# Performance work log

Hardware: AMD Instinct MI355X
Metric: run time of the kernel (lower is better)

## Reference

```python
import math
import jax, jax.numpy as jnp
import numpy as np

B, S, D, H, HD = 2, 2048, 1024, 16, 64  # batch, seq, dim, heads, head_dim
EPS = 1e-5

def setup_inputs() -> dict:
    key = jax.random.key(0)
    ks = jax.random.split(key, 10)
    init = lambda k, shape: jax.random.normal(k, shape, jnp.float32) * 0.02
    return {
        "x": jax.random.normal(ks[0], (B, S, D), jnp.float32),
        "cos": jax.random.uniform(ks[1], (1, S, 1, 1, HD), dtype=jnp.float32),
        "sin": jax.random.uniform(ks[2], (1, S, 1, 1, HD), dtype=jnp.float32),
        "c": jax.random.normal(ks[3], (B, D), jnp.float32),
        "norm1_w": jnp.ones((D,), jnp.float32),
        "w_qkv": init(ks[4], (3 * D, D)),
        "w_out": init(ks[5], (D, D)),
        "norm2_w": jnp.ones((D,), jnp.float32),
        "mlp_w1": init(ks[6], (4 * D, D)),
        "mlp_b1": jnp.zeros((4 * D,), jnp.float32),
        "mlp_w2": init(ks[7], (D, 4 * D)),
        "mlp_b2": jnp.zeros((D,), jnp.float32),
        "ada_w": init(ks[8], (6 * D, D)),
        "ada_b": init(ks[9], (6 * D,)),
    }

def _ln(x, w):
    # LayerNorm computed in fp32, no bias, then scaled by weight
    xf = x.astype(jnp.float32)
    mu = xf.mean(-1, keepdims=True)
    var = xf.var(-1, keepdims=True)
    return (xf - mu) * jax.lax.rsqrt(var + EPS) * w

def _modulate(h, shift, scale):
    return h * (1.0 + scale[:, None, :]) + shift[:, None, :]

def reference(x, cos, sin, c, norm1_w, w_qkv, w_out, norm2_w,
              mlp_w1, mlp_b1, mlp_w2, mlp_b2, ada_w, ada_b):
    # adaLN modulation params: [B, 6D] -> six [B, D] chunks
    ada = c @ ada_w.T + ada_b
    sh_msa, sc_msa, g_msa, sh_mlp, sc_mlp, g_mlp = jnp.split(ada, 6, axis=-1)

    # attention branch (flash_attn path: no rotary applied, naive full softmax)
    h = _modulate(_ln(x, norm1_w), sh_msa, sc_msa)
    qkv = (h @ w_qkv.T).reshape(B, S, 3, H, HD)
    q, k, v = qkv[:, :, 0], qkv[:, :, 1], qkv[:, :, 2]
    scores = jnp.einsum('bqhd,bkhd->bhqk', q, k) / math.sqrt(HD)
    probs = jax.nn.softmax(scores, axis=-1)
    attn = jnp.einsum('bhqk,bkhd->bqhd', probs, v).reshape(B, S, D)
    # gate * dropout(out) + residual; eval mode -> dropout = identity
    x = x + g_msa[:, None, :] * (attn @ w_out.T)

    # MLP branch
    h = _modulate(_ln(x, norm2_w), sh_mlp, sc_mlp)
    h = jax.nn.gelu(h @ mlp_w1.T + mlp_b1, approximate=True) @ mlp_w2.T + mlp_b2
    return x + g_mlp[:, None, :] * h
```

## Files before the change

### kernel.cpp

```cpp
#include <hip/hip_runtime.h>
#include <stdint.h>

typedef __attribute__((ext_vector_type(4))) float f32x4;
typedef __attribute__((ext_vector_type(8))) __bf16 bf16x8;

#define DEV static __device__ __forceinline__

DEV unsigned short f2bf(float f){
    uint32_t u = __float_as_uint(f);
    u += 0x7FFFu + ((u >> 16) & 1u);
    return (unsigned short)(u >> 16);
}
DEV float bf2f(unsigned short s){
    uint32_t u = ((uint32_t)s) << 16;
    return __uint_as_float(u);
}

typedef __attribute__((address_space(1))) const void as1v;
typedef __attribute__((address_space(3))) void as3v;
DEV void g2l16(const void* g, void* l){
    __builtin_amdgcn_global_load_lds((as1v*)g, (as3v*)l, 16, 0, 0);
}

__global__ __launch_bounds__(256) void k_cast_bf16(const float* __restrict__ in,
                                                   unsigned short* __restrict__ out, int n4){
    int i = blockIdx.x * 256 + threadIdx.x;
    if (i < n4){
        float4 v = ((const float4*)in)[i];
        ((ushort4*)out)[i] = make_ushort4(f2bf(v.x), f2bf(v.y), f2bf(v.z), f2bf(v.w));
    }
}

__global__ __launch_bounds__(256) void k_ada(const float* __restrict__ c,
                                             const float* __restrict__ aw,
                                             const float* __restrict__ ab,
                                             float* __restrict__ out){
    int wid  = blockIdx.x * 4 + (threadIdx.x >> 6);
    int lane = threadIdx.x & 63;
    int b = wid / 6144, r = wid % 6144;
    const float4* cw = (const float4*)(c + (size_t)b * 1024);
    const float4* wr = (const float4*)(aw + (size_t)r * 1024);
    float s = 0.f;
    #pragma unroll
    for (int i = 0; i < 4; i++){
        float4 a = wr[lane + i * 64];
        float4 q = cw[lane + i * 64];
        s += a.x*q.x + a.y*q.y + a.z*q.z + a.w*q.w;
    }
    #pragma unroll
    for (int off = 32; off > 0; off >>= 1) s += __shfl_down(s, off);
    if (lane == 0) out[wid] = s + ab[r];
}

__global__ __launch_bounds__(256) void k_ln_mod(const float* __restrict__ x,
                                                const float* __restrict__ w,
                                                const float* __restrict__ ada,
                                                int sh_off, int sc_off,
                                                unsigned short* __restrict__ out){
    int row = blockIdx.x;
    int b   = row >> 11;
    int tid = threadIdx.x;
    float4 v = ((const float4*)(x + (size_t)row * 1024))[tid];
    float s  = v.x + v.y + v.z + v.w;
    float ss = v.x*v.x + v.y*v.y + v.z*v.z + v.w*v.w;
    #pragma unroll
    for (int off = 32; off > 0; off >>= 1){ s += __shfl_down(s, off); ss += __shfl_down(ss, off); }
    __shared__ float red[8];
    int wv = tid >> 6;
    if ((tid & 63) == 0){ red[wv] = s; red[4 + wv] = ss; }
    __syncthreads();
    float S  = red[0] + red[1] + red[2] + red[3];
    float SS = red[4] + red[5] + red[6] + red[7];
    float mu   = S * (1.f / 1024.f);
    float rstd = rsqrtf(SS * (1.f / 1024.f) - mu * mu + 1e-5f);
    const float* adab = ada + (size_t)b * 6144;
    float4 wv4 = ((const float4*)w)[tid];
    float4 sh  = ((const float4*)(adab + sh_off))[tid];
    float4 sc  = ((const float4*)(adab + sc_off))[tid];
    float h0 = (v.x - mu) * rstd * wv4.x * (1.f + sc.x) + sh.x;
    float h1 = (v.y - mu) * rstd * wv4.y * (1.f + sc.y) + sh.y;
    float h2 = (v.z - mu) * rstd * wv4.z * (1.f + sc.z) + sh.z;
    float h3 = (v.w - mu) * rstd * wv4.w * (1.f + sc.w) + sh.w;
    ((ushort4*)(out + (size_t)row * 1024))[tid] = make_ushort4(f2bf(h0), f2bf(h1), f2bf(h2), f2bf(h3));
}

template<int MODE>
__global__ __launch_bounds__(256) void k_gemm(const unsigned short* __restrict__ A,
                                              const unsigned short* __restrict__ B,
                                              void* __restrict__ outp,
                                              const float* __restrict__ bias,
                                              const float* __restrict__ res,
                                              const float* __restrict__ ada, int goff,
                                              int M, int N, int K){
    __shared__ unsigned short As[2 * 128 * 32];
    __shared__ unsigned short Bs[2 * 128 * 32];
    int tid = threadIdx.x, lane = tid & 63, wv = tid >> 6;
    int quad = lane >> 4, l15 = lane & 15;
    int wm = wv & 1, wn = wv >> 1;
    int bm = blockIdx.x, bn = blockIdx.y;
    int klo, khi;
    if constexpr (MODE == 3){
        klo = blockIdx.z * 1376;
        khi = klo + 1376; if (khi > K) khi = K;
    } else {
        int kpb = K / gridDim.z;
        klo = blockIdx.z * kpb; khi = klo + kpb;
    }
    f32x4 acc[4][4] = {};
    int srow = wv * 16 + (lane >> 2), sseg = lane & 3;
    const unsigned short* ga = A + (size_t)(bm * 128 + srow) * K + sseg * 8;
    const unsigned short* gb = B + (size_t)(bn * 128 + srow) * K + sseg * 8;
    size_t stride64 = (size_t)64 * K;
    int wb = wv * 512;
    g2l16(ga + klo,            As + wb);
    g2l16(ga + stride64 + klo, As + 2048 + wb);
    g2l16(gb + klo,            Bs + wb);
    g2l16(gb + stride64 + klo, Bs + 2048 + wb);
    for (int k0 = klo; k0 < khi; k0 += 32){
        int cur = ((k0 - klo) >> 5) & 1;
        unsigned short* as = As + cur * 4096;
        unsigned short* bs = Bs + cur * 4096;
        __syncthreads();
        if (k0 + 32 < khi){
            unsigned short* an = As + (cur ^ 1) * 4096;
            unsigned short* bn = Bs + (cur ^ 1) * 4096;
            g2l16(ga + k0 + 32,            an + wb);
            g2l16(ga + stride64 + k0 + 32, an + 2048 + wb);
            g2l16(gb + k0 + 32,            bn + wb);
            g2l16(gb + stride64 + k0 + 32, bn + 2048 + wb);
        }
        bf16x8 af[4], bfr[4];
        #pragma unroll
        for (int i = 0; i < 4; i++)
            af[i] = *(const bf16x8*)(as + (wm * 64 + i * 16 + l15) * 32 + quad * 8);
        #pragma unroll
        for (int j = 0; j < 4; j++)
            bfr[j] = *(const bf16x8*)(bs + (wn * 64 + j * 16 + l15) * 32 + quad * 8);
        #pragma unroll
        for (int i = 0; i < 4; i++)
            #pragma unroll
            for (int j = 0; j < 4; j++)
                acc[i][j] = __builtin_amdgcn_mfma_f32_16x16x32_bf16(af[i], bfr[j], acc[i][j], 0, 0, 0);
    }
    unsigned short* zp = nullptr;
    if constexpr (MODE == 3){
        int z = blockIdx.z;
        if (z < 2) zp = (unsigned short*)outp + (size_t)z * 4194304;
        else       zp = (unsigned short*)(void*)bias;
    }
    int row0 = bm * 128 + wm * 64, col0 = bn * 128 + wn * 64;
    #pragma unroll
    for (int i = 0; i < 4; i++){
        #pragma unroll
        for (int r = 0; r < 4; r++){
            int row = row0 + i * 16 + quad * 4 + r;
            #pragma unroll
            for (int j = 0; j < 4; j++){
                int col = col0 + j * 16 + l15;
                float v = acc[i][j][r];
                size_t idx = (size_t)row * N + col;
                if constexpr (MODE == 0){
                    ((unsigned short*)outp)[idx] = f2bf(v);
                } else if constexpr (MODE == 1){
                    float t = v + bias[col];
                    float u = 1.5957691216057308f * (t + 0.044715f * t * t * t);
                    float g = t / (1.f + __expf(-u));
                    ((unsigned short*)outp)[idx] = f2bf(g);
                } else if constexpr (MODE == 2){
                    float t = v;
                    if (bias) t += bias[col];
                    int bb = row >> 11;
                    float g = ada[(size_t)bb * 6144 + goff + col];
                    ((float*)outp)[idx] = res[idx] + g * t;
                } else {
                    zp[idx] = f2bf(v);
                }
            }
        }
    }
}

__global__ __launch_bounds__(256) void k_ep2(const unsigned short* __restrict__ z01,
                                             const unsigned short* __restrict__ z2,
                                             const float* __restrict__ bias,
                                             const float* __restrict__ res,
                                             const float* __restrict__ ada, int goff,
                                             float* __restrict__ out){
    int row = blockIdx.x;
    int bb  = row >> 11;
    int tid = threadIdx.x;
    size_t base = (size_t)row * 1024 + tid * 4;
    ushort4 a0 = *(const ushort4*)(z01 + base);
    ushort4 a1 = *(const ushort4*)(z01 + 4194304 + base);
    ushort4 a2 = *(const ushort4*)(z2 + base);
    float4 rv = *(const float4*)(res + base);
    float4 bv = ((const float4*)bias)[tid];
    float4 gv = ((const float4*)(ada + (size_t)bb * 6144 + goff))[tid];
    float4 o;
    o.x = rv.x + gv.x * (bf2f(a0.x) + bf2f(a1.x) + bf2f(a2.x) + bv.x);
    o.y = rv.y + gv.y * (bf2f(a0.y) + bf2f(a1.y) + bf2f(a2.y) + bv.y);
    o.z = rv.z + gv.z * (bf2f(a0.z) + bf2f(a1.z) + bf2f(a2.z) + bv.z);
    o.w = rv.w + gv.w * (bf2f(a0.w) + bf2f(a1.w) + bf2f(a2.w) + bv.w);
    *(float4*)(out + base) = o;
}

__global__ __launch_bounds__(256) void k_vt(const unsigned short* __restrict__ qkv,
                                            unsigned short* __restrict__ vt){
    __shared__ unsigned short T[64 * 66];
    int kb = blockIdx.x, bh = blockIdx.y;
    int b = bh >> 4, h = bh & 15;
    size_t rb = (size_t)b * 2048;
    int t = threadIdx.x;
    int key = t >> 2, seg = t & 3;
    const unsigned short* src = qkv + (rb + kb * 64 + key) * 3072 + 2048 + h * 64;
    uint4 v0 = *(const uint4*)(src + seg * 8);
    uint4 v1 = *(const uint4*)(src + 32 + seg * 8);
    const unsigned short* p0 = (const unsigned short*)&v0;
    const unsigned short* p1 = (const unsigned short*)&v1;
    unsigned short* tr = T + key * 66;
    ushort2* t0 = (ushort2*)(tr + seg * 8);
    ushort2* t1 = (ushort2*)(tr + 32 + seg * 8);
    #pragma unroll
    for (int j = 0; j < 4; j++){
        t0[j] = make_ushort2(p0[2*j], p0[2*j+1]);
        t1[j] = make_ushort2(p1[2*j], p1[2*j+1]);
    }
    __syncthreads();
    int d = t >> 2, kseg = t & 3;
    unsigned short obuf[16];
    #pragma unroll
    for (int j = 0; j < 16; j++) obuf[j] = T[(kseg * 16 + j) * 66 + d];
    uint4* dst = (uint4*)(vt + ((size_t)bh * 64 + d) * 2048 + kb * 64 + kseg * 16);
    dst[0] = ((const uint4*)obuf)[0];
    dst[1] = ((const uint4*)obuf)[1];
}

__global__ __launch_bounds__(256) void k_attn(const unsigned short* __restrict__ qkv,
                                              const unsigned short* __restrict__ vt,
                                              unsigned short* __restrict__ out){
    __shared__ unsigned short Ks[2 * 4096];
    __shared__ unsigned short Vs[2 * 4096];
    __shared__ __align__(16) unsigned short Ps[4 * 32 * 72];
    int tid = threadIdx.x, lane = tid & 63, wv = tid >> 6;
    int quad = lane >> 4, l15 = lane & 15;
    int qt = blockIdx.x, bh = blockIdx.y;
    int b = bh >> 4, h = bh & 15;
    size_t rb = (size_t)b * 2048;

    bf16x8 qb[2][2];
    #pragma unroll
    for (int t = 0; t < 2; t++){
        int qrow = qt * 128 + wv * 32 + t * 16 + l15;
        const unsigned short* qp = qkv + ((rb + qrow) * 3072 + h * 64 + quad * 8);
        qb[t][0] = *(const bf16x8*)qp;
        qb[t][1] = *(const bf16x8*)(qp + 32);
    }
    float lsum[2] = {0.f, 0.f};
    f32x4 o[2][4];
    #pragma unroll
    for (int t = 0; t < 2; t++)
        #pragma unroll
        for (int dt = 0; dt < 4; dt++) o[t][dt] = (f32x4){0.f, 0.f, 0.f, 0.f};

    int rr = wv * 16 + (lane >> 2), cs = lane & 3;
    const unsigned short* gk = qkv + (rb + rr) * 3072 + 1024 + h * 64 + cs * 8;
    const unsigned short* gv = vt + ((size_t)bh * 64 + rr) * 2048 + cs * 8;
    int soff = rr * 32 + (cs ^ ((rr >> 1) & 3)) * 8;
    int rsl = (quad ^ ((l15 >> 1) & 3)) * 8;
    unsigned short* Pw = Ps + wv * 32 * 72;

    uint4 rk0 = *(const uint4*)(gk);
    uint4 rk1 = *(const uint4*)(gk + 32);
    uint4 rv0 = *(const uint4*)(gv);
    uint4 rv1 = *(const uint4*)(gv + 32);

    for (int k0 = 0; k0 < 2048; k0 += 64){
        unsigned short* ks = Ks + ((k0 >> 6) & 1) * 4096;
        unsigned short* vs = Vs + ((k0 >> 6) & 1) * 4096;
        int kn = (k0 + 64 < 2048) ? (k0 + 64) : k0;
        uint4 nk0 = *(const uint4*)(gk + (size_t)kn * 3072);
        uint4 nk1 = *(const uint4*)(gk + (size_t)kn * 3072 + 32);
        uint4 nv0 = *(const uint4*)(gv + kn);
        uint4 nv1 = *(const uint4*)(gv + kn + 32);
        *(uint4*)(ks + soff)        = rk0;
        *(uint4*)(ks + 2048 + soff) = rk1;
        *(uint4*)(vs + soff)        = rv0;
        *(uint4*)(vs + 2048 + soff) = rv1;
        __syncthreads();
        rk0 = nk0; rk1 = nk1; rv0 = nv0; rv1 = nv1;
        f32x4 c[2][4];
        #pragma unroll
        for (int kt = 0; kt < 4; kt++){
            bf16x8 ka0 = *(const bf16x8*)(ks + (kt * 16 + l15) * 32 + rsl);
            bf16x8 ka1 = *(const bf16x8*)(ks + 2048 + (kt * 16 + l15) * 32 + rsl);
            #pragma unroll
            for (int t = 0; t < 2; t++){
                f32x4 z = (f32x4){0.f, 0.f, 0.f, 0.f};
                z = __builtin_amdgcn_mfma_f32_16x16x32_bf16(ka0, qb[t][0], z, 0, 0, 0);
                z = __builtin_amdgcn_mfma_f32_16x16x32_bf16(ka1, qb[t][1], z, 0, 0, 0);
                c[t][kt] = z;
            }
        }
        #pragma unroll
        for (int t = 0; t < 2; t++){
            #pragma unroll
            for (int kt = 0; kt < 4; kt++){
                float p0 = __expf(c[t][kt][0] * 0.125f);
                float p1 = __expf(c[t][kt][1] * 0.125f);
                float p2 = __expf(c[t][kt][2] * 0.125f);
                float p3 = __expf(c[t][kt][3] * 0.125f);
                lsum[t] += (p0 + p1) + (p2 + p3);
                union { uint2 u; __bf16 bh4[4]; } w;
                w.bh4[0] = (__bf16)p0;
                w.bh4[1] = (__bf16)p1;
                w.bh4[2] = (__bf16)p2;
                w.bh4[3] = (__bf16)p3;
                *(uint2*)(Pw + (t * 16 + l15) * 72 + kt * 16 + quad * 4) = w.u;
            }
        }
        bf16x8 pa[2][2];
        #pragma unroll
        for (int t = 0; t < 2; t++){
            pa[t][0] = *(const bf16x8*)(Pw + (t * 16 + l15) * 72 + quad * 8);
            pa[t][1] = *(const bf16x8*)(Pw + (t * 16 + l15) * 72 + 32 + quad * 8);
        }
        #pragma unroll
        for (int dt = 0; dt < 4; dt++){
            bf16x8 vb0 = *(const bf16x8*)(vs + (dt * 16 + l15) * 32 + rsl);
            bf16x8 vb1 = *(const bf16x8*)(vs + 2048 + (dt * 16 + l15) * 32 + rsl);
            #pragma unroll
            for (int t = 0; t < 2; t++){
                o[t][dt] = __builtin_amdgcn_mfma_f32_16x16x32_bf16(pa[t][0], vb0, o[t][dt], 0, 0, 0);
                o[t][dt] = __builtin_amdgcn_mfma_f32_16x16x32_bf16(pa[t][1], vb1, o[t][dt], 0, 0, 0);
            }
        }
    }
    #pragma unroll
    for (int t = 0; t < 2; t++){
        lsum[t] += __shfl_xor(lsum[t], 16);
        lsum[t] += __shfl_xor(lsum[t], 32);
    }
    #pragma unroll
    for (int t = 0; t < 2; t++){
        #pragma unroll
        for (int r = 0; r < 4; r++){
            float lt = __shfl(lsum[t], quad * 4 + r);
            float inv = 1.f / lt;
            int row = qt * 128 + wv * 32 + t * 16 + quad * 4 + r;
            unsigned short* op = out + ((rb + row) * 1024 + h * 64);
            #pragma unroll
            for (int dt = 0; dt < 4; dt++)
                op[dt * 16 + l15] = f2bf(o[t][dt][r] * inv);
        }
    }
}

extern "C" void kernel_launch(void* const* d_in, const int* in_sizes, int n_in,
                              void* d_out, int out_size, void* d_ws, size_t ws_size,
                              hipStream_t stream){
    const float* x     = (const float*)d_in[0];
    const float* c     = (const float*)d_in[3];
    const float* n1w   = (const float*)d_in[4];
    const float* w_qkv = (const float*)d_in[5];
    const float* w_out = (const float*)d_in[6];
    const float* n2w   = (const float*)d_in[7];
    const float* w1    = (const float*)d_in[8];
    const float* b1    = (const float*)d_in[9];
    const float* w2    = (const float*)d_in[10];
    const float* b2    = (const float*)d_in[11];
    const float* ada_w = (const float*)d_in[12];
    const float* ada_b = (const float*)d_in[13];
    float* out = (float*)d_out;
    char* ws = (char*)d_ws;

    unsigned short* wqkv_b = (unsigned short*)(ws + 0);
    unsigned short* wout_b = (unsigned short*)(ws + 6291456);
    unsigned short* w1_b   = (unsigned short*)(ws + 8388608);
    unsigned short* w2_b   = (unsigned short*)(ws + 16777216);
    float*          ada    = (float*)         (ws + 25165824);
    unsigned short* h      = (unsigned short*)(ws + 25214976);
    unsigned short* qkv    = (unsigned short*)(ws + 33603584);
    unsigned short* attn   = (unsigned short*)(ws + 58769408);
    float*          xn     = (float*)         (ws + 67158016);
    unsigned short* u      = qkv;
    unsigned short* vt     = h;
    unsigned short* z01 = (unsigned short*)(ws + 0);
    unsigned short* z2  = (unsigned short*)(ws + 25214976);

    k_cast_bf16<<<3072, 256, 0, stream>>>(w_qkv, wqkv_b,  786432);
    k_cast_bf16<<<1024, 256, 0, stream>>>(w_out, wout_b,  262144);
    k_cast_bf16<<<4096, 256, 0, stream>>>(w1,    w1_b,   1048576);
    k_cast_bf16<<<4096, 256, 0, stream>>>(w2,    w2_b,   1048576);
    k_ada<<<3072, 256, 0, stream>>>(c, ada_w, ada_b, ada);
    k_ln_mod<<<4096, 256, 0, stream>>>(x, n1w, ada, 0, 1024, h);
    k_gemm<0><<<dim3(32, 24), 256, 0, stream>>>(h, wqkv_b, qkv, nullptr, nullptr, nullptr, 0, 4096, 3072, 1024);
    k_vt<<<dim3(32, 32), 256, 0, stream>>>(qkv, vt);
    k_attn<<<dim3(16, 32), 256, 0, stream>>>(qkv, vt, attn);
    k_gemm<2><<<dim3(32, 8), 256, 0, stream>>>(attn, wout_b, xn, nullptr, x, ada, 2048, 4096, 1024, 1024);
    k_ln_mod<<<4096, 256, 0, stream>>>(xn, n2w, ada, 3072, 4096, h);
    k_gemm<1><<<dim3(32, 32), 256, 0, stream>>>(h, w1_b, u, b1, nullptr, nullptr, 0, 4096, 4096, 1024);
    k_gemm<3><<<dim3(32, 8, 3), 256, 0, stream>>>(u, w2_b, z01, (const float*)z2, nullptr,
                                                  nullptr, 0, 4096, 1024, 4096);
    k_ep2<<<4096, 256, 0, stream>>>(z01, z2, b2, xn, ada, 5120, out);
}
```

Before: 394.5 us.

## Triple-buffer GEMM LDS staging with explicit vmcnt waits

Replaces the double-buffered global-to-LDS pipeline in the GEMM kernel with a three-stage ring, issuing loads two K-tiles ahead. Explicit s_waitcnt vmcnt counts and raw s_barrier calls replace __syncthreads, so only the current tile's loads must land before compute. The aim is to hide more global memory latency behind MFMA work. The cost is 50% more LDS per block, which may reduce occupancy, plus hand-tuned wait counts that are fragile if the load count per stage changes.

```diff
diff --git a/kernel.cpp b/kernel.cpp
--- a/kernel.cpp
+++ b/kernel.cpp
@@ -92,8 +92,8 @@
                                               const float* __restrict__ res,
                                               const float* __restrict__ ada, int goff,
                                               int M, int N, int K){
-    __shared__ unsigned short As[2 * 128 * 32];
-    __shared__ unsigned short Bs[2 * 128 * 32];
+    __shared__ unsigned short As[3 * 4096];
+    __shared__ unsigned short Bs[3 * 4096];
     int tid = threadIdx.x, lane = tid & 63, wv = tid >> 6;
     int quad = lane >> 4, l15 = lane & 15;
     int wm = wv & 1, wn = wv >> 1;
@@ -112,23 +112,32 @@
     const unsigned short* gb = B + (size_t)(bn * 128 + srow) * K + sseg * 8;
     size_t stride64 = (size_t)64 * K;
     int wb = wv * 512;
-    g2l16(ga + klo,            As + wb);
-    g2l16(ga + stride64 + klo, As + 2048 + wb);
-    g2l16(gb + klo,            Bs + wb);
-    g2l16(gb + stride64 + klo, Bs + 2048 + wb);
-    for (int k0 = klo; k0 < khi; k0 += 32){
-        int cur = ((k0 - klo) >> 5) & 1;
-        unsigned short* as = As + cur * 4096;
-        unsigned short* bs = Bs + cur * 4096;
-        __syncthreads();
-        if (k0 + 32 < khi){
-            unsigned short* an = As + (cur ^ 1) * 4096;
-            unsigned short* bn = Bs + (cur ^ 1) * 4096;
-            g2l16(ga + k0 + 32,            an + wb);
-            g2l16(ga + stride64 + k0 + 32, an + 2048 + wb);
-            g2l16(gb + k0 + 32,            bn + wb);
-            g2l16(gb + stride64 + k0 + 32, bn + 2048 + wb);
-        }
+    int nt = (khi - klo) >> 5;
+    auto STAGE = [&](int t, int bufi){
+        unsigned short* as = As + bufi * 4096;
+        unsigned short* bs = Bs + bufi * 4096;
+        int ko = klo + (t << 5);
+        g2l16(ga + ko,            as + wb);
+        g2l16(ga + stride64 + ko, as + 2048 + wb);
+        g2l16(gb + ko,            bs + wb);
+        g2l16(gb + stride64 + ko, bs + 2048 + wb);
+    };
+    STAGE(0, 0);
+    STAGE(1, 1);
+    for (int t = 0; t < nt; ++t){
+        int bi = t % 3;
+        if (t){
+            __builtin_amdgcn_s_barrier();
+            __builtin_amdgcn_sched_barrier(0);
+        }
+        if (t + 2 < nt) STAGE(t + 2, (t + 2) % 3);
+        if (t + 2 < nt)      asm volatile("s_waitcnt vmcnt(8)" ::: "memory");
+        else if (t + 1 < nt) asm volatile("s_waitcnt vmcnt(4)" ::: "memory");
+        else                 asm volatile("s_waitcnt vmcnt(0)" ::: "memory");
+        __builtin_amdgcn_s_barrier();
+        __builtin_amdgcn_sched_barrier(0);
+        const unsigned short* as = As + bi * 4096;
+        const unsigned short* bs = Bs + bi * 4096;
         bf16x8 af[4], bfr[4];
         #pragma unroll
         for (int i = 0; i < 4; i++)
```

Result: no change. 395.0 us (+0.1%).

## Split attention KV range across two blocks, combine partial outputs, fold scale into Q weights

Applied to the files above, without the earlier changes.

Attention now launches twice as many blocks, each covering half of the key sequence and writing unnormalized bf16 partial outputs plus row sums. A new combine kernel adds the two halves and normalizes them. The softmax scale and log2(e) are folded into the Q weight cast so exp2 can be used directly, and row sums are computed with MFMA against a ones vector instead of scalar adds. The goal is higher occupancy for the 512-block attention grid, at the cost of an extra pass and extra memory traffic. No max subtraction is done, so overflow risk stays as before, and the bf16 partials add rounding error.

```diff
diff --git a/kernel.cpp b/kernel.cpp
--- a/kernel.cpp
+++ b/kernel.cpp
@@ -28,6 +28,17 @@
     if (i < n4){
         float4 v = ((const float4*)in)[i];
         ((ushort4*)out)[i] = make_ushort4(f2bf(v.x), f2bf(v.y), f2bf(v.z), f2bf(v.w));
+    }
+}
+
+__global__ __launch_bounds__(256) void k_cast_bf16q(const float* __restrict__ in,
+                                                    unsigned short* __restrict__ out,
+                                                    int n4, int nq4){
+    int i = blockIdx.x * 256 + threadIdx.x;
+    if (i < n4){
+        float4 v = ((const float4*)in)[i];
+        float s = (i < nq4) ? 0.18033688011112043f : 1.f;
+        ((ushort4*)out)[i] = make_ushort4(f2bf(v.x * s), f2bf(v.y * s), f2bf(v.z * s), f2bf(v.w * s));
     }
 }
 
@@ -103,8 +114,7 @@
         klo = blockIdx.z * 1376;
         khi = klo + 1376; if (khi > K) khi = K;
     } else {
-        int kpb = K / gridDim.z;
-        klo = blockIdx.z * kpb; khi = klo + kpb;
+        klo = 0; khi = K;
     }
     f32x4 acc[4][4] = {};
     int srow = wv * 16 + (lane >> 2), sseg = lane & 3;
@@ -123,11 +133,11 @@
         __syncthreads();
         if (k0 + 32 < khi){
             unsigned short* an = As + (cur ^ 1) * 4096;
-            unsigned short* bn = Bs + (cur ^ 1) * 4096;
+            unsigned short* bn2 = Bs + (cur ^ 1) * 4096;
             g2l16(ga + k0 + 32,            an + wb);
             g2l16(ga + stride64 + k0 + 32, an + 2048 + wb);
-            g2l16(gb + k0 + 32,            bn + wb);
-            g2l16(gb + stride64 + k0 + 32, bn + 2048 + wb);
+            g2l16(gb + k0 + 32,            bn2 + wb);
+            g2l16(gb + stride64 + k0 + 32, bn2 + 2048 + wb);
         }
         bf16x8 af[4], bfr[4];
         #pragma unroll
@@ -237,15 +247,17 @@
 
 __global__ __launch_bounds__(256) void k_attn(const unsigned short* __restrict__ qkv,
                                               const unsigned short* __restrict__ vt,
-                                              unsigned short* __restrict__ out){
+                                              unsigned short* __restrict__ oh,
+                                              float* __restrict__ lsb){
     __shared__ unsigned short Ks[2 * 4096];
     __shared__ unsigned short Vs[2 * 4096];
     __shared__ __align__(16) unsigned short Ps[4 * 32 * 72];
     int tid = threadIdx.x, lane = tid & 63, wv = tid >> 6;
     int quad = lane >> 4, l15 = lane & 15;
-    int qt = blockIdx.x, bh = blockIdx.y;
+    int qt = blockIdx.x, bh = blockIdx.y, kvh = blockIdx.z;
     int b = bh >> 4, h = bh & 15;
     size_t rb = (size_t)b * 2048;
+    int klo2 = kvh << 10, kend = klo2 + 1024;
 
     bf16x8 qb[2][2];
     #pragma unroll
@@ -255,7 +267,10 @@
         qb[t][0] = *(const bf16x8*)qp;
         qb[t][1] = *(const bf16x8*)(qp + 32);
     }
-    float lsum[2] = {0.f, 0.f};
+    bf16x8 ONES;
+    #pragma unroll
+    for (int i = 0; i < 8; i++) ONES[i] = (__bf16)1.0f;
+    f32x4 ls[2] = {};
     f32x4 o[2][4];
     #pragma unroll
     for (int t = 0; t < 2; t++)
@@ -269,15 +284,15 @@
     int rsl = (quad ^ ((l15 >> 1) & 3)) * 8;
     unsigned short* Pw = Ps + wv * 32 * 72;
 
-    uint4 rk0 = *(const uint4*)(gk);
-    uint4 rk1 = *(const uint4*)(gk + 32);
-    uint4 rv0 = *(const uint4*)(gv);
-    uint4 rv1 = *(const uint4*)(gv + 32);
-
-    for (int k0 = 0; k0 < 2048; k0 += 64){
+    uint4 rk0 = *(const uint4*)(gk + (size_t)klo2 * 3072);
+    uint4 rk1 = *(const uint4*)(gk + (size_t)klo2 * 3072 + 32);
+    uint4 rv0 = *(const uint4*)(gv + klo2);
+    uint4 rv1 = *(const uint4*)(gv + klo2 + 32);
+
+    for (int k0 = klo2; k0 < kend; k0 += 64){
         unsigned short* ks = Ks + ((k0 >> 6) & 1) * 4096;
         unsigned short* vs = Vs + ((k0 >> 6) & 1) * 4096;
-        int kn = (k0 + 64 < 2048) ? (k0 + 64) : k0;
+        int kn = (k0 + 64 < kend) ? (k0 + 64) : k0;
         uint4 nk0 = *(const uint4*)(gk + (size_t)kn * 3072);
         uint4 nk1 = *(const uint4*)(gk + (size_t)kn * 3072 + 32);
         uint4 nv0 = *(const uint4*)(gv + kn);
@@ -305,11 +320,10 @@
         for (int t = 0; t < 2; t++){
             #pragma unroll
             for (int kt = 0; kt < 4; kt++){
-                float p0 = __expf(c[t][kt][0] * 0.125f);
-                float p1 = __expf(c[t][kt][1] * 0.125f);
-                float p2 = __expf(c[t][kt][2] * 0.125f);
-                float p3 = __expf(c[t][kt][3] * 0.125f);
-                lsum[t] += (p0 + p1) + (p2 + p3);
+                float p0 = __builtin_amdgcn_exp2f(c[t][kt][0]);
+                float p1 = __builtin_amdgcn_exp2f(c[t][kt][1]);
+                float p2 = __builtin_amdgcn_exp2f(c[t][kt][2]);
+                float p3 = __builtin_amdgcn_exp2f(c[t][kt][3]);
                 union { uint2 u; __bf16 bh4[4]; } w;
                 w.bh4[0] = (__bf16)p0;
                 w.bh4[1] = (__bf16)p1;
@@ -325,6 +339,11 @@
             pa[t][1] = *(const bf16x8*)(Pw + (t * 16 + l15) * 72 + 32 + quad * 8);
         }
         #pragma unroll
+        for (int t = 0; t < 2; t++){
+            ls[t] = __builtin_amdgcn_mfma_f32_16x16x32_bf16(pa[t][0], ONES, ls[t], 0, 0, 0);
+            ls[t] = __builtin_amdgcn_mfma_f32_16x16x32_bf16(pa[t][1], ONES, ls[t], 0, 0, 0);
+        }
+        #pragma unroll
         for (int dt = 0; dt < 4; dt++){
             bf16x8 vb0 = *(const bf16x8*)(vs + (dt * 16 + l15) * 32 + rsl);
             bf16x8 vb1 = *(const bf16x8*)(vs + 2048 + (dt * 16 + l15) * 32 + rsl);
@@ -335,24 +354,40 @@
             }
         }
     }
+    unsigned short* ohh = oh + (size_t)kvh * 4194304;
+    float* lsh = lsb + (size_t)kvh * 65536;
     #pragma unroll
     for (int t = 0; t < 2; t++){
-        lsum[t] += __shfl_xor(lsum[t], 16);
-        lsum[t] += __shfl_xor(lsum[t], 32);
-    }
-    #pragma unroll
-    for (int t = 0; t < 2; t++){
         #pragma unroll
         for (int r = 0; r < 4; r++){
-            float lt = __shfl(lsum[t], quad * 4 + r);
-            float inv = 1.f / lt;
             int row = qt * 128 + wv * 32 + t * 16 + quad * 4 + r;
-            unsigned short* op = out + ((rb + row) * 1024 + h * 64);
+            size_t grow = rb + row;
+            unsigned short* op = ohh + (grow * 1024 + h * 64);
             #pragma unroll
             for (int dt = 0; dt < 4; dt++)
-                op[dt * 16 + l15] = f2bf(o[t][dt][r] * inv);
-        }
-    }
+                op[dt * 16 + l15] = f2bf(o[t][dt][r]);
+            if (l15 == 0) lsh[grow * 16 + h] = ls[t][r];
+        }
+    }
+}
+
+__global__ __launch_bounds__(256) void k_cmb(const unsigned short* __restrict__ oh,
+                                             const float* __restrict__ lsb,
+                                             unsigned short* __restrict__ out){
+    int row = blockIdx.x;
+    int tid = threadIdx.x;
+    int col = tid * 4;
+    int h = col >> 6;
+    size_t base = (size_t)row * 1024 + col;
+    ushort4 a = *(const ushort4*)(oh + base);
+    ushort4 b = *(const ushort4*)(oh + 4194304 + base);
+    float inv = 1.f / (lsb[row * 16 + h] + lsb[65536 + row * 16 + h]);
+    ushort4 o;
+    o.x = f2bf((bf2f(a.x) + bf2f(b.x)) * inv);
+    o.y = f2bf((bf2f(a.y) + bf2f(b.y)) * inv);
+    o.z = f2bf((bf2f(a.z) + bf2f(b.z)) * inv);
+    o.w = f2bf((bf2f(a.w) + bf2f(b.w)) * inv);
+    *(ushort4*)(out + base) = o;
 }
 
 extern "C" void kernel_launch(void* const* d_in, const int* in_sizes, int n_in,
@@ -384,10 +419,12 @@
     float*          xn     = (float*)         (ws + 67158016);
     unsigned short* u      = qkv;
     unsigned short* vt     = h;
+    unsigned short* oh  = (unsigned short*)(ws + 67158016);
+    float*          lsb = (float*)         (ws + 0);
     unsigned short* z01 = (unsigned short*)(ws + 0);
     unsigned short* z2  = (unsigned short*)(ws + 25214976);
 
-    k_cast_bf16<<<3072, 256, 0, stream>>>(w_qkv, wqkv_b,  786432);
+    k_cast_bf16q<<<3072, 256, 0, stream>>>(w_qkv, wqkv_b, 786432, 262144);
     k_cast_bf16<<<1024, 256, 0, stream>>>(w_out, wout_b,  262144);
     k_cast_bf16<<<4096, 256, 0, stream>>>(w1,    w1_b,   1048576);
     k_cast_bf16<<<4096, 256, 0, stream>>>(w2,    w2_b,   1048576);
@@ -395,7 +432,8 @@
     k_ln_mod<<<4096, 256, 0, stream>>>(x, n1w, ada, 0, 1024, h);
     k_gemm<0><<<dim3(32, 24), 256, 0, stream>>>(h, wqkv_b, qkv, nullptr, nullptr, nullptr, 0, 4096, 3072, 1024);
     k_vt<<<dim3(32, 32), 256, 0, stream>>>(qkv, vt);
-    k_attn<<<dim3(16, 32), 256, 0, stream>>>(qkv, vt, attn);
+    k_attn<<<dim3(16, 32, 2), 256, 0, stream>>>(qkv, vt, oh, lsb);
+    k_cmb<<<4096, 256, 0, stream>>>(oh, lsb, attn);
     k_gemm<2><<<dim3(32, 8), 256, 0, stream>>>(attn, wout_b, xn, nullptr, x, ada, 2048, 4096, 1024, 1024);
     k_ln_mod<<<4096, 256, 0, stream>>>(xn, n2w, ada, 3072, 4096, h);
     k_gemm<1><<<dim3(32, 32), 256, 0, stream>>>(h, w1_b, u, b1, nullptr, nullptr, 0, 4096, 4096, 1024);
```

Result: slower. 402.6 us (+2.0%).
